# Kernel tuning notes

Hardware: AMD Instinct MI355X
Metric: run time of the kernel (lower is better)

The kernel has to match this reference:

```python
import jax, jax.numpy as jnp
import numpy as np

C_IN = 128      # in_channels == num_hiddens (required for residual add)
C_RES = 64      # num_residual_hiddens
D = 512         # representation_dim (in == out)


def _complete_conv1d(x, W, Wc, bc):
    """Faithful fused form of CompleteConv1d.forward for batch=1.

    x:  (1, C, D)   input
    W:  (C, D, D)   stacked per-channel Linear weights (W[c] maps D->D)
    Wc: (OC, C)     1x1 Conv1d weight (kernel dim squeezed)
    bc: (OC,)       1x1 Conv1d bias

    The autograd jacobian of the per-channel linear map is block diagonal:
      xy_grad[c, o, c', i] = W[c, o, i] * delta(c, c')
    so xy_grad_reduced[o, i] = sum_c W[c, o, i], node[i] = argmax_o of that,
    and the python double loop is a scatter-add:
      (y - y_neg)[0, f, n] = sum_{i : node[i]==n} W[f, n, i] * x[0, f, i]
    (y itself, including the Linear biases, cancels exactly).
    """
    d = W.shape[1]
    node = jnp.argmax(jnp.sum(W, axis=0), axis=0)          # (D,) argmax over o
    idx = jnp.arange(d)
    vals = W[:, node, idx] * x[0]                           # (C, D): W[f,node[i],i]*x[0,f,i]
    diff = jnp.zeros_like(x[0]).at[:, node].add(vals)       # scatter-add over repeated nodes
    out = jnp.einsum('oc,cd->od', Wc, diff) + bc[:, None]   # 1x1 conv == channel GEMM
    return out[None]                                        # (1, OC, D)


def setup_inputs() -> dict:
    key = jax.random.key(0)
    ks = jax.random.split(key, 7)
    s = lambda k, shape, scale: (jax.random.normal(k, shape, dtype=jnp.float32) * scale)
    return {
        'x':   s(ks[0], (1, C_IN, D), 1.0),
        'W1':  s(ks[1], (C_IN, D, D), D ** -0.5),
        'Wc1': s(ks[2], (C_RES, C_IN), C_IN ** -0.5),
        'bc1': s(ks[3], (C_RES,), 0.02),
        'W2':  s(ks[4], (C_RES, D, D), D ** -0.5),
        'Wc2': s(ks[5], (C_IN, C_RES), C_RES ** -0.5),
        'bc2': s(ks[6], (C_IN,), 0.02),
    }


def reference(x, W1, Wc1, bc1, W2, Wc2, bc2):
    # nn.ReLU(True) inside the Sequential mutates x in place, so the residual
    # add uses relu(x), not x.
    xr = jax.nn.relu(x)
    h1 = _complete_conv1d(xr, W1, Wc1, bc1)
    h2 = _complete_conv1d(jax.nn.relu(h1), W2, Wc2, bc2)
    return xr + h2
```

## Files before the change

kernel.cpp:

```cpp
#include <hip/hip_runtime.h>

#define C_IN  128
#define C_RES 64
#define D     512
#define DD    (D * D)
#define NC4   (DD / 4)

__device__ __forceinline__ float4 colsum64(const float4* __restrict__ p) {
    float4 acc = make_float4(0.f, 0.f, 0.f, 0.f);
#pragma unroll 16
    for (int c = 0; c < 64; ++c) {
        float4 w = p[(size_t)c * NC4];
        acc.x += w.x; acc.y += w.y; acc.z += w.z; acc.w += w.w;
    }
    return acc;
}

__global__ __launch_bounds__(256)
void sum_init_kernel(const float* __restrict__ W1,
                     const float* __restrict__ W2,
                     const float* __restrict__ x,
                     const float* __restrict__ bc2,
                     float* __restrict__ S1lo,
                     float* __restrict__ S1hi,
                     float* __restrict__ S2,
                     float* __restrict__ diff1,
                     float* __restrict__ out) {
    const int u = blockIdx.x * 256 + threadIdx.x;
    if (u < NC4) {
        ((float4*)S1lo)[u] = colsum64((const float4*)W1 + u);
    } else {
        int t = u - NC4;
        ((float4*)S1hi)[t] = colsum64((const float4*)W1 + (size_t)64 * NC4 + t);
    }
    if (u < NC4 / 2) {
        int t = u + NC4 / 2;
        ((float4*)S1hi)[t] = colsum64((const float4*)W1 + (size_t)64 * NC4 + t);
    } else {
        int t = u - NC4 / 2;
        ((float4*)S2)[t] = colsum64((const float4*)W2 + t);
    }
    if (u < C_IN * D) {
        diff1[u] = 0.f;
        out[u] = fmaxf(x[u], 0.f) + bc2[u >> 9];
    }
}

__global__ __launch_bounds__(256)
void argmax_scatter_kernel(const float* __restrict__ S1lo,
                           const float* __restrict__ S1hi,
                           const float* __restrict__ S2,
                           const float* __restrict__ W1,
                           const float* __restrict__ W2,
                           const float* __restrict__ x,
                           float* __restrict__ diff1,
                           float* __restrict__ w2v,
                           int* __restrict__ node2) {
    __shared__ float lv[256];
    __shared__ int   li[256];
    __shared__ int   node_s[16];

    const int  tid = threadIdx.x;
    const bool st1 = blockIdx.x < 32;
    const int  i0  = (blockIdx.x & 31) * 16;
    const int  il  = tid & 15;
    const int  ol  = tid >> 4;

    float best = -__builtin_inff();
    int   bidx = D;
#pragma unroll 4
    for (int k = 0; k < 32; ++k) {
        int o   = ol + (k << 4);
        int off = o * D + i0 + il;
        float v = st1 ? (S1lo[off] + S1hi[off]) : S2[off];
        if (v > best) { best = v; bidx = o; }
    }
    lv[tid] = best; li[tid] = bidx;
    __syncthreads();
    for (int s = 128; s >= 16; s >>= 1) {
        if (tid < s) {
            float v2 = lv[tid + s]; int i2 = li[tid + s];
            if (v2 > lv[tid] || (v2 == lv[tid] && i2 < li[tid])) {
                lv[tid] = v2; li[tid] = i2;
            }
        }
        __syncthreads();
    }
    if (tid < 16) {
        node_s[tid] = li[tid];
        if (!st1) node2[i0 + tid] = li[tid];
    }
    __syncthreads();

    if (st1) {
        for (int idx = tid; idx < C_IN * 16; idx += 256) {
            int ii = idx & 15;
            int c  = idx >> 4;
            int i  = i0 + ii;
            int n  = node_s[ii];
            float xv = fmaxf(x[c * D + i], 0.f);
            float w  = W1[(size_t)c * DD + (size_t)n * D + i];
            atomicAdd(&diff1[c * D + n], w * xv);
        }
    } else {
        for (int idx = tid; idx < C_RES * 16; idx += 256) {
            int ii = idx & 15;
            int c  = idx >> 4;
            int i  = i0 + ii;
            int n  = node_s[ii];
            w2v[c * D + i] = W2[(size_t)c * DD + (size_t)n * D + i];
        }
    }
}

__global__ __launch_bounds__(256)
void tail_kernel(const float* __restrict__ Wc1,
                 const float* __restrict__ bc1,
                 const float* __restrict__ diff1,
                 const float* __restrict__ w2v,
                 const int* __restrict__ node2,
                 const float* __restrict__ Wc2,
                 float* __restrict__ out) {
    __shared__ float wc1s[C_RES][C_IN + 1];
    __shared__ float d1s[C_IN][8];
    __shared__ float ts[C_RES][9];
    __shared__ int   nds[8];

    const int tid = threadIdx.x;
    const int i0  = blockIdx.x * 8;

    for (int idx = tid; idx < C_RES * C_IN; idx += 256)
        wc1s[idx >> 7][idx & 127] = Wc1[idx];
    for (int idx = tid; idx < C_IN * 8; idx += 256)
        d1s[idx >> 3][idx & 7] = diff1[(idx >> 3) * D + i0 + (idx & 7)];
    if (tid < 8) nds[tid] = node2[i0 + tid];
    __syncthreads();

    {
        const int c = tid & 63;
        const int j = tid >> 6;
        float a0 = bc1[c];
        float a1 = a0;
#pragma unroll 8
        for (int cc = 0; cc < C_IN; ++cc) {
            float w = wc1s[c][cc];
            a0 += w * d1s[cc][2 * j];
            a1 += w * d1s[cc][2 * j + 1];
        }
        ts[c][2 * j]     = w2v[c * D + i0 + 2 * j]     * fmaxf(a0, 0.f);
        ts[c][2 * j + 1] = w2v[c * D + i0 + 2 * j + 1] * fmaxf(a1, 0.f);
    }
    __syncthreads();

    {
        const int o = tid >> 1;
        const int h = tid & 1;
        float z0 = 0.f, z1 = 0.f, z2 = 0.f, z3 = 0.f;
#pragma unroll 8
        for (int c = 0; c < C_RES; ++c) {
            float w = Wc2[o * C_RES + c];
            z0 += w * ts[c][4 * h];
            z1 += w * ts[c][4 * h + 1];
            z2 += w * ts[c][4 * h + 2];
            z3 += w * ts[c][4 * h + 3];
        }
        atomicAdd(&out[o * D + nds[4 * h]],     z0);
        atomicAdd(&out[o * D + nds[4 * h + 1]], z1);
        atomicAdd(&out[o * D + nds[4 * h + 2]], z2);
        atomicAdd(&out[o * D + nds[4 * h + 3]], z3);
    }
}

extern "C" void kernel_launch(void* const* d_in, const int* in_sizes, int n_in,
                              void* d_out, int out_size, void* d_ws, size_t ws_size,
                              hipStream_t stream) {
    const float* x   = (const float*)d_in[0];
    const float* W1  = (const float*)d_in[1];
    const float* Wc1 = (const float*)d_in[2];
    const float* bc1 = (const float*)d_in[3];
    const float* W2  = (const float*)d_in[4];
    const float* Wc2 = (const float*)d_in[5];
    const float* bc2 = (const float*)d_in[6];
    float* out = (float*)d_out;

    float* ws    = (float*)d_ws;
    float* S1lo  = ws;
    float* S1hi  = S1lo + DD;
    float* S2    = S1hi + DD;
    float* diff1 = S2 + DD;
    float* w2v   = diff1 + C_IN * D;
    int*   node2 = (int*)(w2v + C_RES * D);

    sum_init_kernel<<<384, 256, 0, stream>>>(W1, W2, x, bc2,
                                             S1lo, S1hi, S2, diff1, out);
    argmax_scatter_kernel<<<64, 256, 0, stream>>>(S1lo, S1hi, S2, W1, W2, x,
                                                  diff1, w2v, node2);
    tail_kernel<<<64, 256, 0, stream>>>(Wc1, bc1, diff1, w2v, node2, Wc2, out);
}
```

Baseline: 290.9 us.

## Split channel-sum into 24 partial planes across 1536 blocks for more parallelism

The weight column-sum is restructured so that each block reduces only 8 channels for one tile, writing 24 partial-sum planes (16 for W1, 8 for W2). The argmax kernel then adds the partial planes itself. Grid size goes from 384 to 1536 blocks, giving many more loads in flight so the 50 MB weight read can run closer to HBM bandwidth. In exchange it writes and re-reads about 24 MB of partial sums instead of 3 MB, and the argmax kernel does more memory traffic with only 64 blocks.

New measurement: 296.7 us. No clear change (+2.0%).

```diff
diff --git a/kernel.cpp b/kernel.cpp
--- a/kernel.cpp
+++ b/kernel.cpp
@@ -5,41 +5,51 @@
 #define D     512
 #define DD    (D * D)
 #define NC4   (DD / 4)
-
-__device__ __forceinline__ float4 colsum64(const float4* __restrict__ p) {
-    float4 acc = make_float4(0.f, 0.f, 0.f, 0.f);
-#pragma unroll 16
-    for (int c = 0; c < 64; ++c) {
-        float4 w = p[(size_t)c * NC4];
-        acc.x += w.x; acc.y += w.y; acc.z += w.z; acc.w += w.w;
-    }
-    return acc;
-}
+#define TILE4 1024
 
 __global__ __launch_bounds__(256)
 void sum_init_kernel(const float* __restrict__ W1,
                      const float* __restrict__ W2,
                      const float* __restrict__ x,
                      const float* __restrict__ bc2,
-                     float* __restrict__ S1lo,
-                     float* __restrict__ S1hi,
-                     float* __restrict__ S2,
+                     float* __restrict__ Sp,
                      float* __restrict__ diff1,
                      float* __restrict__ out) {
-    const int u = blockIdx.x * 256 + threadIdx.x;
-    if (u < NC4) {
-        ((float4*)S1lo)[u] = colsum64((const float4*)W1 + u);
+    const int t = threadIdx.x;
+    const int b = blockIdx.x;
+    const float4* __restrict__ src;
+    float4* __restrict__ dst;
+    if (b < 1024) {
+        const int tile = b >> 4, g = b & 15;
+        src = (const float4*)W1 + (size_t)(g * 8) * NC4 + tile * TILE4;
+        dst = (float4*)Sp + (size_t)g * NC4 + tile * TILE4;
     } else {
-        int t = u - NC4;
-        ((float4*)S1hi)[t] = colsum64((const float4*)W1 + (size_t)64 * NC4 + t);
-    }
-    if (u < NC4 / 2) {
-        int t = u + NC4 / 2;
-        ((float4*)S1hi)[t] = colsum64((const float4*)W1 + (size_t)64 * NC4 + t);
-    } else {
-        int t = u - NC4 / 2;
-        ((float4*)S2)[t] = colsum64((const float4*)W2 + t);
-    }
+        const int b2 = b - 1024;
+        const int tile = b2 >> 3, g = b2 & 7;
+        src = (const float4*)W2 + (size_t)(g * 8) * NC4 + tile * TILE4;
+        dst = (float4*)Sp + (size_t)(16 + g) * NC4 + tile * TILE4;
+    }
+    const int o0 = ((t >> 6) << 8) + (t & 63);
+    float4 a0 = make_float4(0.f, 0.f, 0.f, 0.f);
+    float4 a1 = a0, a2 = a0, a3 = a0;
+#pragma unroll
+    for (int cc = 0; cc < 8; ++cc) {
+        const float4* p = src + (size_t)cc * NC4;
+        float4 w0 = p[o0];
+        float4 w1 = p[o0 + 64];
+        float4 w2 = p[o0 + 128];
+        float4 w3 = p[o0 + 192];
+        a0.x += w0.x; a0.y += w0.y; a0.z += w0.z; a0.w += w0.w;
+        a1.x += w1.x; a1.y += w1.y; a1.z += w1.z; a1.w += w1.w;
+        a2.x += w2.x; a2.y += w2.y; a2.z += w2.z; a2.w += w2.w;
+        a3.x += w3.x; a3.y += w3.y; a3.z += w3.z; a3.w += w3.w;
+    }
+    dst[o0]       = a0;
+    dst[o0 + 64]  = a1;
+    dst[o0 + 128] = a2;
+    dst[o0 + 192] = a3;
+
+    const int u = b * 256 + t;
     if (u < C_IN * D) {
         diff1[u] = 0.f;
         out[u] = fmaxf(x[u], 0.f) + bc2[u >> 9];
@@ -47,9 +57,7 @@
 }
 
 __global__ __launch_bounds__(256)
-void argmax_scatter_kernel(const float* __restrict__ S1lo,
-                           const float* __restrict__ S1hi,
-                           const float* __restrict__ S2,
+void argmax_scatter_kernel(const float* __restrict__ Sp,
                            const float* __restrict__ W1,
                            const float* __restrict__ W2,
                            const float* __restrict__ x,
@@ -65,14 +73,21 @@
     const int  i0  = (blockIdx.x & 31) * 16;
     const int  il  = tid & 15;
     const int  ol  = tid >> 4;
+    const float* __restrict__ base = st1 ? Sp : Sp + (size_t)16 * DD;
 
     float best = -__builtin_inff();
     int   bidx = D;
-#pragma unroll 4
     for (int k = 0; k < 32; ++k) {
-        int o   = ol + (k << 4);
-        int off = o * D + i0 + il;
-        float v = st1 ? (S1lo[off] + S1hi[off]) : S2[off];
+        const int o   = ol + (k << 4);
+        const int off = o * D + i0 + il;
+        float v = 0.f;
+        if (st1) {
+#pragma unroll
+            for (int pl = 0; pl < 16; ++pl) v += base[(size_t)pl * DD + off];
+        } else {
+#pragma unroll
+            for (int pl = 0; pl < 8; ++pl)  v += base[(size_t)pl * DD + off];
+        }
         if (v > best) { best = v; bidx = o; }
     }
     lv[tid] = best; li[tid] = bidx;
@@ -184,16 +199,13 @@
     float* out = (float*)d_out;
 
     float* ws    = (float*)d_ws;
-    float* S1lo  = ws;
-    float* S1hi  = S1lo + DD;
-    float* S2    = S1hi + DD;
-    float* diff1 = S2 + DD;
+    float* Sp    = ws;
+    float* diff1 = Sp + (size_t)24 * DD;
     float* w2v   = diff1 + C_IN * D;
     int*   node2 = (int*)(w2v + C_RES * D);
 
-    sum_init_kernel<<<384, 256, 0, stream>>>(W1, W2, x, bc2,
-                                             S1lo, S1hi, S2, diff1, out);
-    argmax_scatter_kernel<<<64, 256, 0, stream>>>(S1lo, S1hi, S2, W1, W2, x,
+    sum_init_kernel<<<1536, 256, 0, stream>>>(W1, W2, x, bc2, Sp, diff1, out);
+    argmax_scatter_kernel<<<64, 256, 0, stream>>>(Sp, W1, W2, x,
                                                   diff1, w2v, node2);
     tail_kernel<<<64, 256, 0, stream>>>(Wc1, bc1, diff1, w2v, node2, Wc2, out);
 }
```
